# Performance work log

Measured on AMD Instinct MI355X. Metric: run time of the kernel, lower is better.

The kernel has to match this reference:

```python
import jax, jax.numpy as jnp
import numpy as np

EPS = 1e-6

def setup_inputs() -> dict:
    key = jax.random.key(0)
    ks = jax.random.split(key, 8)
    B, L, Dm, N, K = 2, 1024, 1024, 64, 4
    Di = Dm * 2  # expand=2
    g = lambda k, shape, scale: jax.random.normal(k, shape, jnp.float32) * scale
    return {
        "x": g(ks[0], (B, L, Dm), 1.0),
        "norm_w": jnp.ones((Dm,), jnp.float32),
        "in_proj_w": g(ks[1], (2 * Di, Dm), 0.02),
        "conv_w": g(ks[2], (Di, 1, K), 0.1),      # depthwise: [out=Di, in/groups=1, K]
        "conv_b": jnp.zeros((Di,), jnp.float32),
        "x_proj_w": g(ks[3], (2 * N, Di), 0.02),
        "dt_w": g(ks[4], (Di, Di), 0.02),
        "dt_b": jnp.ones((Di,), jnp.float32),      # init.constant_(dt_proj.bias, 1.0)
        "A_log": g(ks[5], (Di, N), 1.0) - 4.0,     # normal(mean=-4, std=1)
        "D_param": jnp.ones((Di,), jnp.float32),
        "out_proj_w": g(ks[6], (Dm, Di), 0.02),
    }

def reference(x, norm_w, in_proj_w, conv_w, conv_b, x_proj_w, dt_w, dt_b, A_log, D_param, out_proj_w):
    B, L, Dm = x.shape
    Di = conv_w.shape[0]
    K = conv_w.shape[-1]
    skip = x
    # RMSNorm
    rms = jnp.sqrt(jnp.mean(x * x, axis=-1, keepdims=True) + EPS)
    xn = norm_w * (x / rms)
    # in_proj -> [B,L,2*Di], split into x and res
    xr = xn @ in_proj_w.T
    xi, res = jnp.split(xr, 2, axis=-1)
    # causal depthwise conv1d (pad left K-1, truncate to L == torch pad=K-1 then [:L])
    xc = jax.lax.conv_general_dilated(
        xi.transpose(0, 2, 1), conv_w, window_strides=(1,),
        padding=[(K - 1, 0)], dimension_numbers=("NCH", "OIH", "NCH"),
        feature_group_count=Di)
    xc = (xc + conv_b[None, :, None]).transpose(0, 2, 1)  # [B,L,Di]
    xc = jax.nn.silu(xc)
    # selective scan
    x_dbl = xc @ x_proj_w.T                   # [B,L,2N]; first half (delta) unused, as in source
    _delta, B_ssm = jnp.split(x_dbl, 2, axis=-1)  # B_ssm: [B,L,N]
    dt = jax.nn.softplus(xc @ dt_w.T + dt_b)  # [B,L,Di]
    A = -jnp.exp(A_log.astype(jnp.float32))   # [Di,N]
    N = A.shape[-1]

    def step(h, inp):
        x_t, dt_t, B_t = inp                   # [B,Di],[B,Di],[B,N]
        A_disc = jnp.exp(A[None, :, :] * dt_t[:, :, None])   # [B,Di,N]
        h = A_disc * h + B_t[:, None, :] * x_t[:, :, None]   # [B,Di,N]
        y_t = h.sum(axis=-1) + D_param * x_t                 # [B,Di]
        return h, y_t

    h0 = jnp.zeros((B, Di, N), xc.dtype)
    _, ys = jax.lax.scan(step, h0, (xc.transpose(1, 0, 2), dt.transpose(1, 0, 2), B_ssm.transpose(1, 0, 2)))
    y = ys.transpose(1, 0, 2)                  # [B,L,Di]
    out = (y * jax.nn.silu(res)) @ out_proj_w.T
    return out + skip
```

## Files before the change

### kernel.cpp

```cpp
#include <hip/hip_runtime.h>
#include <hip/hip_bf16.h>
#include <math.h>

#define L_DIM 1024
#define DM 1024
#define DI 2048
#define NS 64

typedef __attribute__((ext_vector_type(8))) short short8;
typedef __attribute__((ext_vector_type(4))) float f32x4;

__device__ __forceinline__ ushort bf16u(float f)
{
    unsigned u = __float_as_uint(f);
    unsigned r = (u + 0x7fffu + ((u >> 16) & 1u)) >> 16;
    return (ushort)r;
}
__device__ __forceinline__ float bf2f(ushort u)
{
    return __uint_as_float((unsigned)u << 16);
}

__device__ __forceinline__ void gld16(const ushort* g, const ushort* l)
{
    __builtin_amdgcn_global_load_lds(
        (const __attribute__((address_space(1))) unsigned int*)g,
        (__attribute__((address_space(3))) unsigned int*)l, 16, 0, 0);
}

__global__ __launch_bounds__(256) void k_rms_xn(const float* __restrict__ x,
    const float* __restrict__ nw, ushort* __restrict__ d)
{
    int row = blockIdx.x;
    const float* xp = x + (size_t)row * DM;
    float4 v = ((const float4*)xp)[threadIdx.x];
    float ss = v.x*v.x + v.y*v.y + v.z*v.z + v.w*v.w;
    #pragma unroll
    for (int m = 32; m; m >>= 1) ss += __shfl_xor(ss, m, 64);
    __shared__ float red[4];
    if ((threadIdx.x & 63) == 0) red[threadIdx.x >> 6] = ss;
    __syncthreads();
    float tot = red[0] + red[1] + red[2] + red[3];
    float ri = rsqrtf(tot * (1.0f / DM) + 1e-6f);
    float4 wv = ((const float4*)nw)[threadIdx.x];
    ((ushort4*)(d + (size_t)row * DM))[threadIdx.x] =
        make_ushort4(bf16u(v.x*ri*wv.x), bf16u(v.y*ri*wv.y),
                     bf16u(v.z*ri*wv.z), bf16u(v.w*ri*wv.w));
}

__device__ __forceinline__ void cast8(const float* __restrict__ s,
                                      ushort* __restrict__ d, int i)
{
    float4 a = ((const float4*)s)[2*i], b = ((const float4*)s)[2*i+1];
    ((ushort4*)d)[2*i]   = make_ushort4(bf16u(a.x), bf16u(a.y), bf16u(a.z), bf16u(a.w));
    ((ushort4*)d)[2*i+1] = make_ushort4(bf16u(b.x), bf16u(b.y), bf16u(b.z), bf16u(b.w));
}
__global__ __launch_bounds__(256) void k_castw(
    const float* __restrict__ s0, ushort* __restrict__ d0,
    const float* __restrict__ s1, ushort* __restrict__ d1,
    const float* __restrict__ s2, ushort* __restrict__ d2,
    const float* __restrict__ s3, ushort* __restrict__ d3)
{
    int i = blockIdx.x * 256 + threadIdx.x;
    if (i < 524288)       cast8(s0, d0, i);
    else if (i < 1048576) cast8(s1, d1, i - 524288);
    else if (i < 1064960) cast8(s2, d2, i - 1048576);
    else                  cast8(s3, d3, i - 1064960);
}

template<int MODE>
__global__ __launch_bounds__(256) void k_mfma(
    const ushort* __restrict__ Abf, const ushort* __restrict__ Bbf0,
    const ushort* __restrict__ Bbf1, float* __restrict__ C0,
    ushort* __restrict__ C0b, float* __restrict__ C1,
    const float* __restrict__ bias, const float* __restrict__ skip,
    int Kdim, int ldc)
{
    __shared__ __align__(16) ushort As[128*64];
    __shared__ __align__(16) ushort Bs[128*64];
    const int t = threadIdx.x, w = t >> 6, lane = t & 63;
    const int nwg = gridDim.x * gridDim.y;
    const int orig = blockIdx.y * gridDim.x + blockIdx.x;
    const int swz = (orig & 7) * (nwg >> 3) + (orig >> 3);
    const int nt = swz % gridDim.x, mt = swz / gridDim.x;
    const int mBase = mt * 128, nBase = nt * 128;
    const bool isXP = (MODE == 1) && (nt == 16);
    const ushort* __restrict__ Bbf = isXP ? Bbf1 : Bbf0;
    const int wr = (w >> 1) * 64, wc = (w & 1) * 64;
    const int sR = lane >> 3;
    const int sK = ((lane & 7) ^ sR) * 8;

    f32x4 acc[4][4];
    #pragma unroll
    for (int i = 0; i < 4; ++i)
        #pragma unroll
        for (int j = 0; j < 4; ++j)
            acc[i][j] = (f32x4){0.f, 0.f, 0.f, 0.f};

    for (int kt = 0; kt < Kdim; kt += 64) {
        #pragma unroll
        for (int s = 0; s < 4; ++s) {
            int tr = w*8 + s*32 + sR;
            gld16(Abf + (size_t)(mBase + tr) * Kdim + kt + sK,
                  As + (w*8 + s*32) * 64);
            int gr = isXP ? (tr < 63 ? tr : 63) : (nBase + tr);
            gld16(Bbf + (size_t)gr * Kdim + kt + sK,
                  Bs + (w*8 + s*32) * 64);
        }
        __syncthreads();
        #pragma unroll
        for (int kk = 0; kk < 2; ++kk) {
            short8 af[4], bfr[4];
            #pragma unroll
            for (int f = 0; f < 4; ++f) {
                int ra = wr + f*16 + (lane & 15);
                int ca = (kk*4 + (lane >> 4)) ^ (ra & 7);
                af[f]  = *(const short8*)(As + ra*64 + ca*8);
                int rb2 = wc + f*16 + (lane & 15);
                int cb2 = (kk*4 + (lane >> 4)) ^ (rb2 & 7);
                bfr[f] = *(const short8*)(Bs + rb2*64 + cb2*8);
            }
            #pragma unroll
            for (int mi = 0; mi < 4; ++mi)
                #pragma unroll
                for (int ni = 0; ni < 4; ++ni)
                    acc[mi][ni] = __builtin_amdgcn_mfma_f32_16x16x32_bf16(
                        af[mi], bfr[ni], acc[mi][ni], 0, 0, 0);
        }
        __syncthreads();
    }

    const int rb = (lane >> 4) * 4, cbl = lane & 15;
    #pragma unroll
    for (int mi = 0; mi < 4; ++mi) {
        #pragma unroll
        for (int ni = 0; ni < 4; ++ni) {
            int ltcol = wc + ni*16 + cbl;
            int col = nBase + ltcol;
            #pragma unroll
            for (int j = 0; j < 4; ++j) {
                int row = mBase + wr + mi*16 + rb + j;
                float v = acc[mi][ni][j];
                if constexpr (MODE == 0) {
                    C0b[(size_t)row * ldc + col] = bf16u(v);
                } else if constexpr (MODE == 1) {
                    if (isXP) {
                        if (ltcol < NS) C1[(size_t)row * NS + ltcol] = v;
                    } else {
                        float z = v + bias[col];
                        C0[(size_t)row * ldc + col] =
                            (z > 20.f) ? z : logf(1.f + expf(z));
                    }
                } else {
                    C0[(size_t)row * ldc + col] = v + skip[(size_t)row * ldc + col];
                }
            }
        }
    }
}

__global__ __launch_bounds__(256) void k_conv(const ushort* __restrict__ xrb,
    const float* __restrict__ cw, const float* __restrict__ cb,
    float* __restrict__ xc, ushort* __restrict__ xcb)
{
    int gid = blockIdx.x * 256 + threadIdx.x;
    int d = (gid & 511) * 4;
    int tt = (gid >> 9) & 1023;
    int b = gid >> 19;
    float4 w[4];
    #pragma unroll
    for (int c = 0; c < 4; ++c) w[c] = *(const float4*)(cw + (size_t)(d + c) * 4);
    float4 acc = *(const float4*)(cb + d);
    const ushort* base = xrb + (size_t)b * L_DIM * (2*DI) + d;
    #pragma unroll
    for (int j = 0; j < 4; ++j) {
        int ti = tt - 3 + j;
        if (ti < 0) continue;
        ushort4 xu = *(const ushort4*)(base + (size_t)ti * (2*DI));
        const float* w0 = (const float*)&w[0];
        const float* w1 = (const float*)&w[1];
        const float* w2 = (const float*)&w[2];
        const float* w3 = (const float*)&w[3];
        acc.x = fmaf(w0[j], bf2f(xu.x), acc.x);
        acc.y = fmaf(w1[j], bf2f(xu.y), acc.y);
        acc.z = fmaf(w2[j], bf2f(xu.z), acc.z);
        acc.w = fmaf(w3[j], bf2f(xu.w), acc.w);
    }
    acc.x = acc.x / (1.f + expf(-acc.x));
    acc.y = acc.y / (1.f + expf(-acc.y));
    acc.z = acc.z / (1.f + expf(-acc.z));
    acc.w = acc.w / (1.f + expf(-acc.w));
    size_t o = (size_t)(b * L_DIM + tt) * DI + d;
    *(float4*)(xc + o) = acc;
    *(ushort4*)(xcb + o) = make_ushort4(bf16u(acc.x), bf16u(acc.y),
                                        bf16u(acc.z), bf16u(acc.w));
}

__global__ __launch_bounds__(256) void k_tr4(const float* __restrict__ dtb,
    float* __restrict__ dtt, const float* __restrict__ xc,
    float* __restrict__ xct)
{
    __shared__ float tile[64][65];
    const int r0 = blockIdx.y * 64, c0 = blockIdx.x * 64;
    const int z = blockIdx.z;
    const float* s;
    float* d;
    if (z < 2) { s = dtb + (size_t)z * L_DIM * DI;       d = dtt + (size_t)z * DI * L_DIM; }
    else       { s = xc  + (size_t)(z-2) * L_DIM * DI;   d = xct + (size_t)(z-2) * DI * L_DIM; }
    const int tx = threadIdx.x & 15, ty = threadIdx.x >> 4;
    #pragma unroll
    for (int p = 0; p < 4; ++p) {
        float4 v = *(const float4*)(s + (size_t)(r0 + ty + p*16) * DI + c0 + tx*4);
        tile[ty + p*16][tx*4+0] = v.x; tile[ty + p*16][tx*4+1] = v.y;
        tile[ty + p*16][tx*4+2] = v.z; tile[ty + p*16][tx*4+3] = v.w;
    }
    __syncthreads();
    #pragma unroll
    for (int p = 0; p < 4; ++p) {
        int oc = ty + p*16;
        float4 v = make_float4(tile[tx*4+0][oc], tile[tx*4+1][oc],
                               tile[tx*4+2][oc], tile[tx*4+3][oc]);
        *(float4*)(d + (size_t)(c0 + oc) * L_DIM + r0 + tx*4) = v;
    }
}

__global__ __launch_bounds__(256) void k_trg(const float* __restrict__ yt,
    const ushort* __restrict__ xrb, ushort* __restrict__ ybf)
{
    __shared__ float tile[64][65];
    const int r0 = blockIdx.y * 64, c0 = blockIdx.x * 64;
    const int z = blockIdx.z;
    const float* s = yt + (size_t)z * DI * L_DIM;
    const int tx = threadIdx.x & 15, ty = threadIdx.x >> 4;
    #pragma unroll
    for (int p = 0; p < 4; ++p) {
        float4 v = *(const float4*)(s + (size_t)(r0 + ty + p*16) * L_DIM + c0 + tx*4);
        tile[ty + p*16][tx*4+0] = v.x; tile[ty + p*16][tx*4+1] = v.y;
        tile[ty + p*16][tx*4+2] = v.z; tile[ty + p*16][tx*4+3] = v.w;
    }
    __syncthreads();
    #pragma unroll
    for (int p = 0; p < 4; ++p) {
        int oc = ty + p*16;
        int row = z * L_DIM + c0 + oc;
        float4 v = make_float4(tile[tx*4+0][oc], tile[tx*4+1][oc],
                               tile[tx*4+2][oc], tile[tx*4+3][oc]);
        ushort4 gu = *(const ushort4*)(xrb + (size_t)row * (2*DI) + DI + r0 + tx*4);
        float gx = bf2f(gu.x), gy = bf2f(gu.y), gz = bf2f(gu.z), gw = bf2f(gu.w);
        v.x *= gx / (1.f + expf(-gx));
        v.y *= gy / (1.f + expf(-gy));
        v.z *= gz / (1.f + expf(-gz));
        v.w *= gw / (1.f + expf(-gw));
        *(ushort4*)(ybf + (size_t)row * DI + r0 + tx*4) =
            make_ushort4(bf16u(v.x), bf16u(v.y), bf16u(v.z), bf16u(v.w));
    }
}

__device__ __forceinline__ float rl(float v, int lane)
{
    return __int_as_float(__builtin_amdgcn_readlane(__float_as_int(v), lane));
}
__device__ __forceinline__ float exp2_fast(float x)
{
    float r;
    asm("v_exp_f32 %0, %1" : "=v"(r) : "v"(x));
    return r;
}

__global__ __launch_bounds__(256) void k_scan9(const float* __restrict__ dtt,
    const float* __restrict__ xct, const float* __restrict__ Bss,
    const float* __restrict__ A_log, const float* __restrict__ Dp,
    float* __restrict__ yt)
{
    __shared__ float Bsh[64][68];
    __shared__ __align__(16) float Psh[4][64][4];
    const int lane = threadIdx.x & 63;
    const int widx = threadIdx.x >> 6;
    const int b = blockIdx.x >> 9;
    const int d = (blockIdx.x & 511) * 4 + widx;
    const float aL2 = -expf(A_log[(size_t)d * NS + lane]) * 1.44269504f;
    const float Dv = Dp[d];
    const float* dtp = dtt + ((size_t)b * DI + d) * L_DIM;
    const float* xcp = xct + ((size_t)b * DI + d) * L_DIM;
    const float* Bp  = Bss + (size_t)b * L_DIM * NS;
    float* yp = yt + ((size_t)b * DI + d) * L_DIM;
    const int lr = threadIdx.x >> 2;
    const int lc = (threadIdx.x & 3) * 16;
    const int pg = lane >> 4;
    const bool pwrite = (lane & 15) == 15;
    float h = 0.f;

    for (int t0 = 0; t0 < L_DIM; t0 += 64) {
        const float* bsrc = Bp + (size_t)(t0 + lr) * NS + lc;
        float4 b0 = *(const float4*)(bsrc);
        float4 b1 = *(const float4*)(bsrc + 4);
        float4 b2 = *(const float4*)(bsrc + 8);
        float4 b3 = *(const float4*)(bsrc + 12);
        float dt_v = dtp[t0 + lane];
        float xc_v = xcp[t0 + lane];
        __syncthreads();
        *(float4*)&Bsh[lr][lc]      = b0;
        *(float4*)&Bsh[lr][lc + 4]  = b1;
        *(float4*)&Bsh[lr][lc + 8]  = b2;
        *(float4*)&Bsh[lr][lc + 12] = b3;
        __syncthreads();
        #pragma unroll
        for (int q = 0; q < 64; q += 4) {
            float Bv0 = Bsh[q+0][lane];
            float Bv1 = Bsh[q+1][lane];
            float Bv2 = Bsh[q+2][lane];
            float Bv3 = Bsh[q+3][lane];
            float s0, s1, s2, s3;
            {
                float p, ad;
                p  = rl(xc_v, q+0) * Bv0;
                ad = exp2_fast(aL2 * rl(dt_v, q+0));
                h = fmaf(ad, h, p); s0 = h;
                p  = rl(xc_v, q+1) * Bv1;
                ad = exp2_fast(aL2 * rl(dt_v, q+1));
                h = fmaf(ad, h, p); s1 = h;
                p  = rl(xc_v, q+2) * Bv2;
                ad = exp2_fast(aL2 * rl(dt_v, q+2));
                h = fmaf(ad, h, p); s2 = h;
                p  = rl(xc_v, q+3) * Bv3;
                ad = exp2_fast(aL2 * rl(dt_v, q+3));
                h = fmaf(ad, h, p); s3 = h;
            }
            asm("v_add_f32_dpp %0, %0, %0 row_shr:1 row_mask:0xf bank_mask:0xf\n\t"
                "v_add_f32_dpp %1, %1, %1 row_shr:1 row_mask:0xf bank_mask:0xf\n\t"
                "v_add_f32_dpp %2, %2, %2 row_shr:1 row_mask:0xf bank_mask:0xf\n\t"
                "v_add_f32_dpp %3, %3, %3 row_shr:1 row_mask:0xf bank_mask:0xf\n\t"
                "v_add_f32_dpp %0, %0, %0 row_shr:2 row_mask:0xf bank_mask:0xf\n\t"
                "v_add_f32_dpp %1, %1, %1 row_shr:2 row_mask:0xf bank_mask:0xf\n\t"
                "v_add_f32_dpp %2, %2, %2 row_shr:2 row_mask:0xf bank_mask:0xf\n\t"
                "v_add_f32_dpp %3, %3, %3 row_shr:2 row_mask:0xf bank_mask:0xf\n\t"
                "v_add_f32_dpp %0, %0, %0 row_shr:4 row_mask:0xf bank_mask:0xf\n\t"
                "v_add_f32_dpp %1, %1, %1 row_shr:4 row_mask:0xf bank_mask:0xf\n\t"
                "v_add_f32_dpp %2, %2, %2 row_shr:4 row_mask:0xf bank_mask:0xf\n\t"
                "v_add_f32_dpp %3, %3, %3 row_shr:4 row_mask:0xf bank_mask:0xf\n\t"
                "v_add_f32_dpp %0, %0, %0 row_shr:8 row_mask:0xf bank_mask:0xf\n\t"
                "v_add_f32_dpp %1, %1, %1 row_shr:8 row_mask:0xf bank_mask:0xf\n\t"
                "v_add_f32_dpp %2, %2, %2 row_shr:8 row_mask:0xf bank_mask:0xf\n\t"
                "v_add_f32_dpp %3, %3, %3 row_shr:8 row_mask:0xf bank_mask:0xf"
                : "+v"(s0), "+v"(s1), "+v"(s2), "+v"(s3));
            if (pwrite) {
                Psh[widx][q+0][pg] = s0;
                Psh[widx][q+1][pg] = s1;
                Psh[widx][q+2][pg] = s2;
                Psh[widx][q+3][pg] = s3;
            }
        }
        asm volatile("s_waitcnt lgkmcnt(0)" ::: "memory");
        __builtin_amdgcn_sched_barrier(0);
        float4 pv = *(const float4*)&Psh[widx][lane][0];
        yp[t0 + lane] = fmaf(Dv, xc_v, (pv.x + pv.y) + (pv.z + pv.w));
    }
}

extern "C" void kernel_launch(void* const* d_in, const int* in_sizes, int n_in,
                              void* d_out, int out_size, void* d_ws, size_t ws_size,
                              hipStream_t stream)
{
    const float* x        = (const float*)d_in[0];
    const float* norm_w   = (const float*)d_in[1];
    const float* in_projw = (const float*)d_in[2];
    const float* conv_w   = (const float*)d_in[3];
    const float* conv_b   = (const float*)d_in[4];
    const float* x_projw  = (const float*)d_in[5];
    const float* dt_w     = (const float*)d_in[6];
    const float* dt_b     = (const float*)d_in[7];
    const float* A_log    = (const float*)d_in[8];
    const float* D_param  = (const float*)d_in[9];
    const float* out_projw= (const float*)d_in[10];
    float* out = (float*)d_out;

    float* ws = (float*)d_ws;
    ushort* xr_bf = (ushort*)ws;
    float* xc   = ws + (size_t)4*1024*1024;
    float* dtb  = xc + (size_t)4*1024*1024;
    float* Bss  = dtb + (size_t)4*1024*1024;
    float* dtt  = Bss + 131072;
    float* xct  = dtt + (size_t)4*1024*1024;
    ushort* xn_bf  = (ushort*)(xct + (size_t)4*1024*1024);
    ushort* xc_bf  = xn_bf + (size_t)2*1024*1024;
    ushort* xpw_bf = xc_bf + (size_t)4*1024*1024;
    ushort* opw_bf = xpw_bf + 131072;
    ushort* inpw_bf = (ushort*)dtt;
    ushort* dtw_bf  = (ushort*)xct;
    ushort* y_bf    = (ushort*)xc;
    float* yt = dtb;

    k_castw<<<5184, 256, 0, stream>>>(in_projw, inpw_bf, dt_w, dtw_bf,
                                      x_projw + (size_t)64*2048, xpw_bf,
                                      out_projw, opw_bf);
    k_rms_xn<<<2048, 256, 0, stream>>>(x, norm_w, xn_bf);
    k_mfma<0><<<dim3(32, 16), 256, 0, stream>>>(xn_bf, inpw_bf, nullptr,
                                                nullptr, xr_bf, nullptr,
                                                nullptr, nullptr, 1024, 4096);
    k_conv<<<4096, 256, 0, stream>>>(xr_bf, conv_w, conv_b, xc, xc_bf);
    k_mfma<1><<<dim3(17, 16), 256, 0, stream>>>(xc_bf, dtw_bf, xpw_bf,
                                                dtb, nullptr, Bss,
                                                dt_b, nullptr, 2048, 2048);
    k_tr4<<<dim3(32, 16, 4), 256, 0, stream>>>(dtb, dtt, xc, xct);
    k_scan9<<<1024, 256, 0, stream>>>(dtt, xct, Bss, A_log, D_param, yt);
    k_trg<<<dim3(16, 32, 2), 256, 0, stream>>>(yt, xr_bf, y_bf);
    k_mfma<2><<<dim3(8, 16), 256, 0, stream>>>(y_bf, opw_bf, nullptr,
                                               out, nullptr, nullptr,
                                               nullptr, x, 2048, 1024);
}
```

Baseline: 273.8 us.

## Use 64-row tiles for out_proj GEMM and shorten scan DPP reduction

Templates the MFMA GEMM on the M tile size and launches the out_proj GEMM with 64x128 tiles, doubling its grid from 128 to 256 workgroups so more CUs stay busy. In the scan kernel, the per-timestep cross-lane reduction stops after row_shr:4, writing eight partial sums per timestep to shared memory instead of four. The final output then sums eight partials per step. This trades one DPP stage per sum for extra LDS writes and reads, and the smaller GEMM tile lowers data reuse per block.

```diff
diff --git a/kernel.cpp b/kernel.cpp
--- a/kernel.cpp
+++ b/kernel.cpp
@@ -68,7 +68,7 @@
     else                  cast8(s3, d3, i - 1064960);
 }
 
-template<int MODE>
+template<int MODE, int BM>
 __global__ __launch_bounds__(256) void k_mfma(
     const ushort* __restrict__ Abf, const ushort* __restrict__ Bbf0,
     const ushort* __restrict__ Bbf1, float* __restrict__ C0,
@@ -76,33 +76,40 @@
     const float* __restrict__ bias, const float* __restrict__ skip,
     int Kdim, int ldc)
 {
-    __shared__ __align__(16) ushort As[128*64];
+    constexpr int NI = (BM == 128) ? 4 : 2;
+    constexpr int SA = BM / 32;
+    __shared__ __align__(16) ushort As[BM*64];
     __shared__ __align__(16) ushort Bs[128*64];
     const int t = threadIdx.x, w = t >> 6, lane = t & 63;
     const int nwg = gridDim.x * gridDim.y;
     const int orig = blockIdx.y * gridDim.x + blockIdx.x;
     const int swz = (orig & 7) * (nwg >> 3) + (orig >> 3);
     const int nt = swz % gridDim.x, mt = swz / gridDim.x;
-    const int mBase = mt * 128, nBase = nt * 128;
+    const int mBase = mt * BM, nBase = nt * 128;
     const bool isXP = (MODE == 1) && (nt == 16);
     const ushort* __restrict__ Bbf = isXP ? Bbf1 : Bbf0;
-    const int wr = (w >> 1) * 64, wc = (w & 1) * 64;
+    const int wr = (BM == 128) ? (w >> 1) * 64 : 0;
+    const int wc = (BM == 128) ? (w & 1) * 64 : w * 32;
     const int sR = lane >> 3;
     const int sK = ((lane & 7) ^ sR) * 8;
 
-    f32x4 acc[4][4];
+    f32x4 acc[4][NI];
     #pragma unroll
     for (int i = 0; i < 4; ++i)
         #pragma unroll
-        for (int j = 0; j < 4; ++j)
+        for (int j = 0; j < NI; ++j)
             acc[i][j] = (f32x4){0.f, 0.f, 0.f, 0.f};
 
     for (int kt = 0; kt < Kdim; kt += 64) {
         #pragma unroll
-        for (int s = 0; s < 4; ++s) {
+        for (int s = 0; s < SA; ++s) {
             int tr = w*8 + s*32 + sR;
             gld16(Abf + (size_t)(mBase + tr) * Kdim + kt + sK,
                   As + (w*8 + s*32) * 64);
+        }
+        #pragma unroll
+        for (int s = 0; s < 4; ++s) {
+            int tr = w*8 + s*32 + sR;
             int gr = isXP ? (tr < 63 ? tr : 63) : (nBase + tr);
             gld16(Bbf + (size_t)gr * Kdim + kt + sK,
                   Bs + (w*8 + s*32) * 64);
@@ -110,12 +117,15 @@
         __syncthreads();
         #pragma unroll
         for (int kk = 0; kk < 2; ++kk) {
-            short8 af[4], bfr[4];
+            short8 af[4], bfr[NI];
             #pragma unroll
             for (int f = 0; f < 4; ++f) {
                 int ra = wr + f*16 + (lane & 15);
                 int ca = (kk*4 + (lane >> 4)) ^ (ra & 7);
-                af[f]  = *(const short8*)(As + ra*64 + ca*8);
+                af[f] = *(const short8*)(As + ra*64 + ca*8);
+            }
+            #pragma unroll
+            for (int f = 0; f < NI; ++f) {
                 int rb2 = wc + f*16 + (lane & 15);
                 int cb2 = (kk*4 + (lane >> 4)) ^ (rb2 & 7);
                 bfr[f] = *(const short8*)(Bs + rb2*64 + cb2*8);
@@ -123,7 +133,7 @@
             #pragma unroll
             for (int mi = 0; mi < 4; ++mi)
                 #pragma unroll
-                for (int ni = 0; ni < 4; ++ni)
+                for (int ni = 0; ni < NI; ++ni)
                     acc[mi][ni] = __builtin_amdgcn_mfma_f32_16x16x32_bf16(
                         af[mi], bfr[ni], acc[mi][ni], 0, 0, 0);
         }
@@ -134,7 +144,7 @@
     #pragma unroll
     for (int mi = 0; mi < 4; ++mi) {
         #pragma unroll
-        for (int ni = 0; ni < 4; ++ni) {
+        for (int ni = 0; ni < NI; ++ni) {
             int ltcol = wc + ni*16 + cbl;
             int col = nBase + ltcol;
             #pragma unroll
@@ -273,7 +283,7 @@
     float* __restrict__ yt)
 {
     __shared__ float Bsh[64][68];
-    __shared__ __align__(16) float Psh[4][64][4];
+    __shared__ __align__(16) float Psh[4][64][8];
     const int lane = threadIdx.x & 63;
     const int widx = threadIdx.x >> 6;
     const int b = blockIdx.x >> 9;
@@ -286,8 +296,8 @@
     float* yp = yt + ((size_t)b * DI + d) * L_DIM;
     const int lr = threadIdx.x >> 2;
     const int lc = (threadIdx.x & 3) * 16;
-    const int pg = lane >> 4;
-    const bool pwrite = (lane & 15) == 15;
+    const int pg = lane >> 3;
+    const bool pwrite = (lane & 7) == 7;
     float h = 0.f;
 
     for (int t0 = 0; t0 < L_DIM; t0 += 64) {
@@ -337,11 +347,7 @@
                 "v_add_f32_dpp %0, %0, %0 row_shr:4 row_mask:0xf bank_mask:0xf\n\t"
                 "v_add_f32_dpp %1, %1, %1 row_shr:4 row_mask:0xf bank_mask:0xf\n\t"
                 "v_add_f32_dpp %2, %2, %2 row_shr:4 row_mask:0xf bank_mask:0xf\n\t"
-                "v_add_f32_dpp %3, %3, %3 row_shr:4 row_mask:0xf bank_mask:0xf\n\t"
-                "v_add_f32_dpp %0, %0, %0 row_shr:8 row_mask:0xf bank_mask:0xf\n\t"
-                "v_add_f32_dpp %1, %1, %1 row_shr:8 row_mask:0xf bank_mask:0xf\n\t"
-                "v_add_f32_dpp %2, %2, %2 row_shr:8 row_mask:0xf bank_mask:0xf\n\t"
-                "v_add_f32_dpp %3, %3, %3 row_shr:8 row_mask:0xf bank_mask:0xf"
+                "v_add_f32_dpp %3, %3, %3 row_shr:4 row_mask:0xf bank_mask:0xf"
                 : "+v"(s0), "+v"(s1), "+v"(s2), "+v"(s3));
             if (pwrite) {
                 Psh[widx][q+0][pg] = s0;
@@ -352,8 +358,11 @@
         }
         asm volatile("s_waitcnt lgkmcnt(0)" ::: "memory");
         __builtin_amdgcn_sched_barrier(0);
-        float4 pv = *(const float4*)&Psh[widx][lane][0];
-        yp[t0 + lane] = fmaf(Dv, xc_v, (pv.x + pv.y) + (pv.z + pv.w));
+        float4 p0 = *(const float4*)&Psh[widx][lane][0];
+        float4 p1 = *(const float4*)&Psh[widx][lane][4];
+        float sum = ((p0.x + p0.y) + (p0.z + p0.w))
+                  + ((p1.x + p1.y) + (p1.z + p1.w));
+        yp[t0 + lane] = fmaf(Dv, xc_v, sum);
     }
 }
 
@@ -394,17 +403,17 @@
                                       x_projw + (size_t)64*2048, xpw_bf,
                                       out_projw, opw_bf);
     k_rms_xn<<<2048, 256, 0, stream>>>(x, norm_w, xn_bf);
-    k_mfma<0><<<dim3(32, 16), 256, 0, stream>>>(xn_bf, inpw_bf, nullptr,
+    k_mfma<0,128><<<dim3(32, 16), 256, 0, stream>>>(xn_bf, inpw_bf, nullptr,
                                                 nullptr, xr_bf, nullptr,
                                                 nullptr, nullptr, 1024, 4096);
     k_conv<<<4096, 256, 0, stream>>>(xr_bf, conv_w, conv_b, xc, xc_bf);
-    k_mfma<1><<<dim3(17, 16), 256, 0, stream>>>(xc_bf, dtw_bf, xpw_bf,
+    k_mfma<1,128><<<dim3(17, 16), 256, 0, stream>>>(xc_bf, dtw_bf, xpw_bf,
                                                 dtb, nullptr, Bss,
                                                 dt_b, nullptr, 2048, 2048);
     k_tr4<<<dim3(32, 16, 4), 256, 0, stream>>>(dtb, dtt, xc, xct);
     k_scan9<<<1024, 256, 0, stream>>>(dtt, xct, Bss, A_log, D_param, yt);
     k_trg<<<dim3(16, 32, 2), 256, 0, stream>>>(yt, xr_bf, y_bf);
-    k_mfma<2><<<dim3(8, 16), 256, 0, stream>>>(y_bf, opw_bf, nullptr,
+    k_mfma<2,64><<<dim3(8, 32), 256, 0, stream>>>(y_bf, opw_bf, nullptr,
                                                out, nullptr, nullptr,
                                                nullptr, x, 2048, 1024);
 }
```

Result: faster. 259.5 us (-5.2%).
